# Optimization experiments

Measured on AMD Instinct MI355X. Metric: run time of the kernel, lower is better.

The kernel has to match this reference:

```python
import jax, jax.numpy as jnp
import numpy as np

K_NEIGHBORS = 16
N_CLASSES = 10


def setup_inputs() -> dict:
    key = jax.random.key(0)
    k1, k2, k3 = jax.random.split(key, 3)
    x = jax.random.normal(k1, (2048, 128), dtype=jnp.float32)
    train_data = jax.random.normal(k2, (100000, 128), dtype=jnp.float32)
    train_labels = jax.random.randint(k3, (100000,), 0, N_CLASSES, dtype=jnp.int64)
    return {"x": x, "train_data": train_data, "train_labels": train_labels}


def reference(x, train_data, train_labels):
    N = x.shape[0]
    x2 = jnp.sum(x * x, axis=1, keepdims=True)            # [N, 1]
    t2 = jnp.sum(train_data * train_data, axis=1)          # [M]
    d2 = x2 + t2[None, :] - 2.0 * (x @ train_data.T)       # [N, M]
    dist = jnp.sqrt(jnp.maximum(d2, 0.0))
    # smallest-k via top_k on negated distances
    neg_d, idx = jax.lax.top_k(-dist, K_NEIGHBORS)         # [N, K]
    d = -neg_d
    labels = train_labels[idx]                              # [N, K]
    # weights == 'distance': inverse distance; rows containing an exact match
    # (inf weight) get a 0/1 indicator vector instead.
    w = 1.0 / d
    inf_mask = jnp.isinf(w)
    inf_row = jnp.any(inf_mask, axis=1, keepdims=True)
    w = jnp.where(inf_row, inf_mask.astype(jnp.float32), w)
    # weighted vote: scatter-add weights into per-class buckets
    rows = jnp.arange(N)[:, None]
    proba = jnp.zeros((N, N_CLASSES), jnp.float32).at[rows, labels].add(w)
    s = jnp.sum(proba, axis=1, keepdims=True)
    s = jnp.where(s == 0.0, 1.0, s)
    proba = proba / s
    pred = jnp.argmax(proba, axis=1)
    return pred, proba
```

## Files before the change

kernel.cpp:

```cpp
#include <hip/hip_runtime.h>
#include <hip/hip_fp16.h>
#include <math.h>

#define M_TRAIN 100000
#define NQ 2048
#define DIM 128
#define KNN 16
#define NCLS 10

#define S_STRIDE 16
#define S_CNT (M_TRAIN / S_STRIDE)
#define S_PAD 6272
#define SCH 49
#define SPC 128
#define TT 64
#define MQ 128
#define QSTR 136

#define CAP 768
#define TBH 50176
#define NTR 128
#define NQT 64
#define MARGIN 3.0f
#define SLACK 7.0f

using bfrag = __attribute__((ext_vector_type(8))) short;
using cfrag = __attribute__((ext_vector_type(4))) float;

__device__ __forceinline__ bool better(float d1, int i1, float d2, int i2) {
    return (d1 < d2) || (d1 == d2 && i1 < i2);
}

__device__ __forceinline__ unsigned pack_bf16(float a, float b) {
    unsigned ua = __float_as_uint(a), ub = __float_as_uint(b);
    ua += 0x7fffu + ((ua >> 16) & 1u);
    ub += 0x7fffu + ((ub >> 16) & 1u);
    return (ua >> 16) | (ub & 0xffff0000u);
}

__device__ __forceinline__ bfrag pack_bf16x8(const float* p) {
    union { unsigned u[4]; bfrag f; } r;
    r.u[0] = pack_bf16(p[0], p[1]);
    r.u[1] = pack_bf16(p[2], p[3]);
    r.u[2] = pack_bf16(p[4], p[5]);
    r.u[3] = pack_bf16(p[6], p[7]);
    return r.f;
}

__device__ __forceinline__ void gload_lds16(const void* g, void* l) {
    __builtin_amdgcn_global_load_lds(
        (const __attribute__((address_space(1))) unsigned int*)g,
        (__attribute__((address_space(3))) unsigned int*)l, 16, 0, 0);
}

__device__ __forceinline__ void ins16(float (&bd)[KNN], float v) {
    if (v < bd[KNN - 1]) {
        bd[KNN - 1] = v;
        #pragma unroll
        for (int j = KNN - 1; j >= 1; --j)
            if (bd[j] < bd[j - 1]) { float t = bd[j]; bd[j] = bd[j - 1]; bd[j - 1] = t; }
    }
}

__global__ void knn_norms(const float* __restrict__ train,
                          const float* __restrict__ x,
                          float* __restrict__ t2, float* __restrict__ x2,
                          int* __restrict__ cnt) {
    int gid = blockIdx.x * blockDim.x + threadIdx.x;
    if (gid < NQ) cnt[gid] = 0;
    int gw = gid >> 6;
    int lane = threadIdx.x & 63;
    if (gw >= M_TRAIN + NQ) return;
    const float* r = (gw < M_TRAIN) ? (train + (size_t)gw * DIM)
                                    : (x + (size_t)(gw - M_TRAIN) * DIM);
    float a = r[lane];
    float b = r[lane + 64];
    float s = a * a + b * b;
    #pragma unroll
    for (int off = 32; off > 0; off >>= 1)
        s += __shfl_down(s, off, 64);
    if (lane == 0) {
        if (gw < M_TRAIN) t2[gw] = s; else x2[gw - M_TRAIN] = s;
    }
}

__global__ __launch_bounds__(256, 3)
void knn_sub_mfma(const float* __restrict__ x, const float* __restrict__ train,
                  const float* __restrict__ t2, const float* __restrict__ x2,
                  __half* __restrict__ dsub) {
    __shared__ short T[TT * QSTR];
    __shared__ float t2h[TT];
    int tid = threadIdx.x;
    int w = tid >> 6, lane = tid & 63;
    int rquad = lane >> 4, rcol = lane & 15;
    int qBase = blockIdx.y * MQ;
    int cBase = blockIdx.x * SPC;

    bfrag A[2][4];
    #pragma unroll
    for (int rt = 0; rt < 2; ++rt) {
        int qr = qBase + w * 32 + rt * 16 + rcol;
        #pragma unroll
        for (int ks = 0; ks < 4; ++ks)
            A[rt][ks] = pack_bf16x8(&x[(size_t)qr * DIM + ks * 32 + rquad * 8]);
    }

    float x2r[2][4];
    #pragma unroll
    for (int rt = 0; rt < 2; ++rt)
        #pragma unroll
        for (int reg = 0; reg < 4; ++reg)
            x2r[rt][reg] = x2[qBase + w * 32 + rt * 16 + rquad * 4 + reg];

    const cfrag zero4 = {0.f, 0.f, 0.f, 0.f};
    for (int t = 0; t < 2; ++t) {
        __syncthreads();
        int sBase = cBase + t * TT;
        #pragma unroll
        for (int it = 0; it < 8; ++it) {
            int f = it * 256 + tid;
            int row = f >> 5, c4 = f & 31;
            int sj = sBase + row;
            bool ok = sj < S_CNT;
            float4 v = ok ? ((const float4*)train)[(size_t)sj * S_STRIDE * (DIM / 4) + c4]
                          : make_float4(0.f, 0.f, 0.f, 0.f);
            uint2 p; p.x = pack_bf16(v.x, v.y); p.y = pack_bf16(v.z, v.w);
            *(uint2*)&T[row * QSTR + c4 * 4] = p;
        }
        if (tid < TT) {
            int sj = sBase + tid;
            t2h[tid] = (sj < S_CNT) ? t2[(size_t)sj * S_STRIDE] : 1e30f;
        }
        __syncthreads();

        cfrag acc[2][4];
        #pragma unroll
        for (int ks = 0; ks < 4; ++ks) {
            bfrag B[4];
            #pragma unroll
            for (int ct = 0; ct < 4; ++ct) {
                int n = ct * 16 + rcol;
                B[ct] = *(const bfrag*)&T[n * QSTR + ks * 32 + rquad * 8];
            }
            #pragma unroll
            for (int rt = 0; rt < 2; ++rt)
                #pragma unroll
                for (int ct = 0; ct < 4; ++ct)
                    acc[rt][ct] = (ks == 0)
                        ? __builtin_amdgcn_mfma_f32_16x16x32_bf16(A[rt][0], B[ct], zero4, 0, 0, 0)
                        : __builtin_amdgcn_mfma_f32_16x16x32_bf16(A[rt][ks], B[ct], acc[rt][ct], 0, 0, 0);
        }

        float th[4];
        #pragma unroll
        for (int ct = 0; ct < 4; ++ct) th[ct] = t2h[ct * 16 + rcol];
        #pragma unroll
        for (int rt = 0; rt < 2; ++rt)
            #pragma unroll
            for (int ct = 0; ct < 4; ++ct)
                #pragma unroll
                for (int reg = 0; reg < 4; ++reg) {
                    float d2 = x2r[rt][reg] + th[ct] - 2.f * acc[rt][ct][reg];
                    int qrow = qBase + w * 32 + rt * 16 + rquad * 4 + reg;
                    int col = sBase + ct * 16 + rcol;
                    dsub[(size_t)qrow * S_PAD + col] = __float2half_rn(d2);
                }
    }
}

__global__ __launch_bounds__(256)
void knn_select(const __half* __restrict__ dsub, float* __restrict__ tau) {
    __shared__ float wk[64];
    int q = blockIdx.x, tid = threadIdx.x;
    int w = tid >> 6, lane = tid & 63;

    float bd[KNN];
    #pragma unroll
    for (int j = 0; j < KNN; ++j) bd[j] = 3.4e38f;

    const uint4* dv = (const uint4*)(dsub + (size_t)q * S_PAD);
    #pragma unroll 1
    for (int v = tid; v < S_PAD / 8; v += 256) {
        uint4 pk = dv[v];
        unsigned wd[4] = {pk.x, pk.y, pk.z, pk.w};
        #pragma unroll
        for (int e = 0; e < 4; ++e) {
            ins16(bd, __half2float(__ushort_as_half((unsigned short)(wd[e] & 0xFFFFu))));
            ins16(bd, __half2float(__ushort_as_half((unsigned short)(wd[e] >> 16))));
        }
    }

    #pragma unroll 1
    for (int sel = 0; sel < KNN; ++sel) {
        float mv = bd[0]; int ml = lane;
        #pragma unroll
        for (int off = 32; off > 0; off >>= 1) {
            float ov = __shfl_down(mv, off, 64);
            int   ol = __shfl_down(ml, off, 64);
            if (ov < mv || (ov == mv && ol < ml)) { mv = ov; ml = ol; }
        }
        mv = __shfl(mv, 0, 64);
        ml = __shfl(ml, 0, 64);
        if (lane == 0) wk[w * KNN + sel] = mv;
        if (lane == ml) {
            #pragma unroll
            for (int j = 0; j < KNN - 1; ++j) bd[j] = bd[j + 1];
            bd[KNN - 1] = 3.4e38f;
        }
    }
    __syncthreads();
    if (tid < 64) {
        float v = wk[tid];
        int rank = 0;
        #pragma unroll 8
        for (int j = 0; j < 64; ++j) {
            float u = wk[j];
            if (u < v || (u == v && j < tid)) ++rank;
        }
        if (rank == KNN - 1) tau[q] = v;
    }
}

__global__ __launch_bounds__(256)
void knn_convert_bf16(const float* __restrict__ train,
                      unsigned int* __restrict__ tb, int rowBase,
                      const float* __restrict__ x,
                      unsigned int* __restrict__ xb) {
    int b = blockIdx.x;
    if (b >= (TBH * 32) / 256) {
        int i = (b - (TBH * 32) / 256) * 256 + threadIdx.x;
        int row = i >> 5, seg = i & 31;
        float4 v = ((const float4*)x)[(size_t)row * (DIM / 4) + seg];
        uint2 p; p.x = pack_bf16(v.x, v.y); p.y = pack_bf16(v.z, v.w);
        ((uint2*)xb)[(size_t)row * 32 + seg] = p;
        return;
    }
    int i = b * 256 + threadIdx.x;
    int row = i >> 5, seg = i & 31;
    int g = rowBase + row;
    float4 v = (g < M_TRAIN)
        ? ((const float4*)train)[(size_t)g * (DIM / 4) + seg]
        : make_float4(0.f, 0.f, 0.f, 0.f);
    uint2 p; p.x = pack_bf16(v.x, v.y); p.y = pack_bf16(v.z, v.w);
    int off = (seg * 8) ^ ((row & 7) << 4);
    *(uint2*)((char*)tb + (size_t)row * 256 + off) = p;
}

__global__ __launch_bounds__(256, 5)
void knn_filter12(const unsigned int* __restrict__ xbb,
                  const short* __restrict__ tbb,
                  const float* __restrict__ t2, const float* __restrict__ x2,
                  const float* __restrict__ tau, int pBase0,
                  int* __restrict__ buf_i, unsigned short* __restrict__ buf_h,
                  int* __restrict__ cnt) {
    __shared__ __align__(16) short T[NTR * DIM];
    int tid = threadIdx.x;
    int w = tid >> 6, lane = tid & 63;
    int rquad = lane >> 4, rcol = lane & 15;

    int bid = blockIdx.x;
    int xcd = bid & 7, r = bid >> 3;
    int qb = r & 31;
    int nch = xcd + 8 * (r >> 5);
    int qBase = qb * NQT;
    int tbase = pBase0 + nch * NTR;

    const char* gsrc = (const char*)tbb + (size_t)nch * NTR * 256 + w * 8192 + lane * 16;
    char* ldst = (char*)T + w * 8192;
    #pragma unroll
    for (int i = 0; i < 8; ++i)
        gload_lds16(gsrc + i * 1024, ldst + i * 1024);

    bfrag A[4];
    int qrow = qBase + w * 16 + rcol;
    const char* xrow = (const char*)xbb + (size_t)qrow * 256;
    #pragma unroll
    for (int ks = 0; ks < 4; ++ks)
        A[ks] = *(const bfrag*)(xrow + ks * 64 + rquad * 16);

    float RC[4], x2q[4];
    #pragma unroll
    for (int reg = 0; reg < 4; ++reg) {
        int q = qBase + w * 16 + rquad * 4 + reg;
        x2q[reg] = x2[q];
        RC[reg] = 0.5f * (x2q[reg] - tau[q] - MARGIN);
    }
    float th[8];
    #pragma unroll
    for (int ct = 0; ct < 8; ++ct)
        th[ct] = 0.5f * t2[tbase + ct * 16 + rcol];
    __syncthreads();

    int swz = (rcol & 7) << 4;
    int cs[4];
    #pragma unroll
    for (int ks = 0; ks < 4; ++ks)
        cs[ks] = (ks * 64 + rquad * 16) ^ swz;

    const cfrag zero4 = {0.f, 0.f, 0.f, 0.f};
    cfrag acc[8];
    #pragma unroll
    for (int ks = 0; ks < 4; ++ks)
        #pragma unroll
        for (int ct = 0; ct < 8; ++ct) {
            const bfrag B = *(const bfrag*)((const char*)T + (ct * 16 + rcol) * 256 + cs[ks]);
            acc[ct] = (ks == 0)
                ? __builtin_amdgcn_mfma_f32_16x16x32_bf16(A[0], B, zero4, 0, 0, 0)
                : __builtin_amdgcn_mfma_f32_16x16x32_bf16(A[ks], B, acc[ct], 0, 0, 0);
        }

    unsigned okm = 0;
    #pragma unroll
    for (int ct = 0; ct < 8; ++ct)
        if (tbase + ct * 16 + rcol < M_TRAIN) okm |= (1u << ct);

    unsigned m8[4];
    #pragma unroll
    for (int reg = 0; reg < 4; ++reg) {
        unsigned m = 0;
        #pragma unroll
        for (int ct = 0; ct < 8; ++ct)
            if (acc[ct][reg] >= RC[reg] + th[ct]) m |= (1u << ct);
        m8[reg] = m & okm;
    }

    int slotR[4];
    #pragma unroll
    for (int reg = 0; reg < 4; ++reg)
        if (m8[reg])
            slotR[reg] = atomicAdd(&cnt[qBase + w * 16 + rquad * 4 + reg],
                                   __popc(m8[reg]));

    #pragma unroll
    for (int reg = 0; reg < 4; ++reg) {
        unsigned m = m8[reg];
        if (m) {
            int q = qBase + w * 16 + rquad * 4 + reg;
            size_t qoff = (size_t)q * CAP;
            int s0 = slotR[reg];
            #pragma unroll
            for (int ct = 0; ct < 8; ++ct)
                if (m & (1u << ct)) {
                    int slot = s0 + __popc(m & ((1u << ct) - 1));
                    if (slot < CAP) {
                        buf_i[qoff + slot] = tbase + ct * 16 + rcol;
                        float d2a = x2q[reg] + 2.f * th[ct] - 2.f * acc[ct][reg];
                        buf_h[qoff + slot] = __half_as_ushort(__float2half_rn(d2a));
                    }
                }
        }
    }
}

__global__ __launch_bounds__(256)
void knn_final(const float* __restrict__ x,
               const float* __restrict__ train,
               const float* __restrict__ t2v,
               const float* __restrict__ x2v,
               const int* __restrict__ buf_i,
               const __half* __restrict__ buf_h,
               const int* __restrict__ cnt,
               const int* __restrict__ labels,
               float* __restrict__ out) {
    __shared__ float sd[CAP];
    __shared__ int   si[CAP];
    __shared__ int   keep[CAP];
    __shared__ float wk[64];
    __shared__ int   kr[KNN];
    __shared__ float sthr;
    __shared__ int   smcnt;
    int q = blockIdx.x;
    int tid = threadIdx.x;
    int w = tid >> 6, lane = tid & 63;
    int grp = lane >> 4, sub = lane & 15;
    int n = cnt[q]; if (n > CAP) n = CAP;
    if (tid == 0) smcnt = 0;
    if (tid < KNN) kr[tid] = -1;

    float av[3];
    #pragma unroll
    for (int j = 0; j < 3; ++j) {
        int i = (w * 3 + j) * 64 + lane;
        av[j] = (i < n) ? __half2float(buf_h[(size_t)q * CAP + i]) : 3.4e38f;
    }
    for (int sel = 0; sel < KNN; ++sel) {
        float mv = av[0]; int mc = (lane << 2);
        if (av[1] < mv) { mv = av[1]; mc = (lane << 2) | 1; }
        if (av[2] < mv) { mv = av[2]; mc = (lane << 2) | 2; }
        #pragma unroll
        for (int off = 32; off > 0; off >>= 1) {
            float ov = __shfl_down(mv, off, 64);
            int   oc = __shfl_down(mc, off, 64);
            if (ov < mv || (ov == mv && oc < mc)) { mv = ov; mc = oc; }
        }
        mv = __shfl(mv, 0, 64);
        mc = __shfl(mc, 0, 64);
        if (lane == 0) wk[w * KNN + sel] = mv;
        if (lane == (mc >> 2)) {
            int j0 = mc & 3;
            if (j0 == 0) av[0] = 3.4e38f;
            else if (j0 == 1) av[1] = 3.4e38f;
            else av[2] = 3.4e38f;
        }
    }
    __syncthreads();
    if (tid < 64) {
        float v = wk[tid];
        int rank = 0;
        #pragma unroll 8
        for (int j = 0; j < 64; ++j) {
            float u = wk[j];
            if (u < v || (u == v && j < tid)) ++rank;
        }
        if (rank == KNN - 1) sthr = v + SLACK;
    }
    __syncthreads();
    float thr = sthr;

    for (int i = tid; i < n; i += 256) {
        float h = __half2float(buf_h[(size_t)q * CAP + i]);
        if (h <= thr) {
            int p = atomicAdd(&smcnt, 1);
            keep[p] = buf_i[(size_t)q * CAP + i];
        }
    }
    __syncthreads();
    int m = smcnt;

    const float4* xq = (const float4*)&x[(size_t)q * DIM + sub * 8];
    float4 qa = xq[0], qb = xq[1];
    float x2l = x2v[q];
    for (int base = 0; base < m; base += 16) {
        int i = base + w * 4 + grp;
        if (i < m) {
            int idx = keep[i];
            const float4* tr = (const float4*)&train[(size_t)idx * DIM + sub * 8];
            float4 ta = tr[0], tb4 = tr[1];
            float s = qa.x * ta.x + qa.y * ta.y + qa.z * ta.z + qa.w * ta.w
                    + qb.x * tb4.x + qb.y * tb4.y + qb.z * tb4.z + qb.w * tb4.w;
            s += __shfl_xor(s, 1, 64);
            s += __shfl_xor(s, 2, 64);
            s += __shfl_xor(s, 4, 64);
            s += __shfl_xor(s, 8, 64);
            if (sub == 0) { sd[i] = x2l + t2v[idx] - 2.f * s; si[i] = idx; }
        }
    }
    __syncthreads();

    for (int i = tid; i < m; i += 256) {
        float d = sd[i]; int ix = si[i];
        int rank = 0;
        for (int j = 0; j < m; ++j)
            if (better(sd[j], si[j], d, ix)) ++rank;
        if (rank < KNN) kr[rank] = i;
    }
    __syncthreads();

    if (tid == 0) {
        bool anyzero = false;
        float dist[KNN]; int kidx[KNN];
        #pragma unroll
        for (int j = 0; j < KNN; ++j) {
            int ii = kr[j];
            if (ii >= 0) {
                dist[j] = sqrtf(fmaxf(sd[ii], 0.f));
                kidx[j] = si[ii];
                if (dist[j] == 0.f) anyzero = true;
            } else { dist[j] = -1.f; kidx[j] = -1; }
        }
        float spr[NCLS];
        #pragma unroll
        for (int c = 0; c < NCLS; ++c) spr[c] = 0.f;
        #pragma unroll
        for (int j = 0; j < KNN; ++j) {
            int idxj = kidx[j];
            if (idxj < 0 || idxj >= M_TRAIN) continue;
            float wgt = anyzero ? (dist[j] == 0.f ? 1.f : 0.f) : 1.f / dist[j];
            spr[labels[idxj]] += wgt;
        }
        float s = 0.f;
        #pragma unroll
        for (int c = 0; c < NCLS; ++c) s += spr[c];
        if (s == 0.f) s = 1.f;
        float inv = 1.f / s;
        float best = -1.f; int bc = 0;
        #pragma unroll
        for (int c = 0; c < NCLS; ++c) {
            float pv = spr[c] * inv;
            out[NQ + (size_t)q * NCLS + c] = pv;
            if (pv > best) { best = pv; bc = c; }
        }
        out[q] = (float)bc;
    }
}

extern "C" void kernel_launch(void* const* d_in, const int* in_sizes, int n_in,
                              void* d_out, int out_size, void* d_ws, size_t ws_size,
                              hipStream_t stream) {
    const float* x      = (const float*)d_in[0];
    const float* train  = (const float*)d_in[1];
    const int*   labels = (const int*)d_in[2];
    float* out = (float*)d_out;

    char* base = (char*)d_ws;
    float*  t2   = (float*)(base);
    float*  x2   = (float*)(base + 401408);
    float*  tau  = (float*)(base + 409600);
    int*    cnt  = (int*)  (base + 417792);
    char*   region = base + 425984;
    __half* dsub = (__half*)region;
    unsigned int* tb = (unsigned int*)region;
    int*    bi   = (int*)(region + 12845056);
    unsigned int* xb = (unsigned int*)(region + 19136512);
    __half* bh   = (__half*)(region + 19660800);

    int nrows = M_TRAIN + NQ;
    knn_norms<<<(nrows * 64 + 255) / 256, 256, 0, stream>>>(train, x, t2, x2, cnt);

    dim3 gs(SCH, NQ / MQ);
    knn_sub_mfma<<<gs, 256, 0, stream>>>(x, train, t2, x2, dsub);

    knn_select<<<NQ, 256, 0, stream>>>(dsub, tau);

    for (int h = 0; h < 2; ++h) {
        int rowBase = h * TBH;
        int cgrid = (TBH * 32) / 256 + (h == 0 ? (NQ * 32) / 256 : 0);
        knn_convert_bf16<<<cgrid, 256, 0, stream>>>(train, tb, rowBase, x, xb);
        knn_filter12<<<(TBH / NTR) * (NQ / NQT), 256, 0, stream>>>(
            xb, (const short*)tb, t2, x2, tau, rowBase, bi, (unsigned short*)bh, cnt);
    }

    knn_final<<<NQ, 256, 0, stream>>>(x, train, t2, x2, bi, bh, cnt, labels, out);
}
```

Before: 374.9 us.

## Fuse bf16 conversion of train tiles into filter kernel, drop staging buffer

Removes the separate train-to-bf16 conversion pass and its two-half staging loop. Each filter block now reads fp32 train rows directly, converts them to bf16 and writes the swizzled layout straight into LDS. A small kernel packs the queries to bf16. This cuts the global write and reread of the converted train copy and several launches. In exchange each train tile is read and converted as fp32 once per query block (32 times), which raises global/L2 traffic and ALU work in the filter prologue.

```diff
diff --git a/kernel.cpp b/kernel.cpp
--- a/kernel.cpp
+++ b/kernel.cpp
@@ -18,7 +18,7 @@
 #define QSTR 136
 
 #define CAP 768
-#define TBH 50176
+#define NTILE 784
 #define NTR 128
 #define NQT 64
 #define MARGIN 3.0f
@@ -45,12 +45,6 @@
     r.u[2] = pack_bf16(p[4], p[5]);
     r.u[3] = pack_bf16(p[6], p[7]);
     return r.f;
-}
-
-__device__ __forceinline__ void gload_lds16(const void* g, void* l) {
-    __builtin_amdgcn_global_load_lds(
-        (const __attribute__((address_space(1))) unsigned int*)g,
-        (__attribute__((address_space(3))) unsigned int*)l, 16, 0, 0);
 }
 
 __device__ __forceinline__ void ins16(float (&bd)[KNN], float v) {
@@ -222,35 +216,18 @@
 }
 
 __global__ __launch_bounds__(256)
-void knn_convert_bf16(const float* __restrict__ train,
-                      unsigned int* __restrict__ tb, int rowBase,
-                      const float* __restrict__ x,
-                      unsigned int* __restrict__ xb) {
-    int b = blockIdx.x;
-    if (b >= (TBH * 32) / 256) {
-        int i = (b - (TBH * 32) / 256) * 256 + threadIdx.x;
-        int row = i >> 5, seg = i & 31;
-        float4 v = ((const float4*)x)[(size_t)row * (DIM / 4) + seg];
-        uint2 p; p.x = pack_bf16(v.x, v.y); p.y = pack_bf16(v.z, v.w);
-        ((uint2*)xb)[(size_t)row * 32 + seg] = p;
-        return;
-    }
-    int i = b * 256 + threadIdx.x;
-    int row = i >> 5, seg = i & 31;
-    int g = rowBase + row;
-    float4 v = (g < M_TRAIN)
-        ? ((const float4*)train)[(size_t)g * (DIM / 4) + seg]
-        : make_float4(0.f, 0.f, 0.f, 0.f);
-    uint2 p; p.x = pack_bf16(v.x, v.y); p.y = pack_bf16(v.z, v.w);
-    int off = (seg * 8) ^ ((row & 7) << 4);
-    *(uint2*)((char*)tb + (size_t)row * 256 + off) = p;
+void knn_pack_x(const float* __restrict__ x, unsigned int* __restrict__ xb) {
+    int gid = blockIdx.x * 256 + threadIdx.x;
+    int row = gid >> 6, lane = gid & 63;
+    float2 v = ((const float2*)x)[(size_t)row * 64 + lane];
+    xb[(size_t)row * 64 + lane] = pack_bf16(v.x, v.y);
 }
 
 __global__ __launch_bounds__(256, 5)
-void knn_filter12(const unsigned int* __restrict__ xbb,
-                  const short* __restrict__ tbb,
+void knn_filter14(const unsigned int* __restrict__ xbb,
+                  const float* __restrict__ train,
                   const float* __restrict__ t2, const float* __restrict__ x2,
-                  const float* __restrict__ tau, int pBase0,
+                  const float* __restrict__ tau,
                   int* __restrict__ buf_i, unsigned short* __restrict__ buf_h,
                   int* __restrict__ cnt) {
     __shared__ __align__(16) short T[NTR * DIM];
@@ -263,13 +240,20 @@
     int qb = r & 31;
     int nch = xcd + 8 * (r >> 5);
     int qBase = qb * NQT;
-    int tbase = pBase0 + nch * NTR;
-
-    const char* gsrc = (const char*)tbb + (size_t)nch * NTR * 256 + w * 8192 + lane * 16;
-    char* ldst = (char*)T + w * 8192;
-    #pragma unroll
-    for (int i = 0; i < 8; ++i)
-        gload_lds16(gsrc + i * 1024, ldst + i * 1024);
+    int tbase = nch * NTR;
+
+    #pragma unroll
+    for (int it = 0; it < 16; ++it) {
+        int f = it * 256 + tid;
+        int row = f >> 5, seg = f & 31;
+        int g = tbase + row;
+        float4 v = (g < M_TRAIN)
+            ? ((const float4*)train)[(size_t)g * (DIM / 4) + seg]
+            : make_float4(0.f, 0.f, 0.f, 0.f);
+        uint2 p; p.x = pack_bf16(v.x, v.y); p.y = pack_bf16(v.z, v.w);
+        int off = (seg * 8) ^ ((row & 7) << 4);
+        *(uint2*)((char*)T + row * 256 + off) = p;
+    }
 
     bfrag A[4];
     int qrow = qBase + w * 16 + rcol;
@@ -509,7 +493,6 @@
     int*    cnt  = (int*)  (base + 417792);
     char*   region = base + 425984;
     __half* dsub = (__half*)region;
-    unsigned int* tb = (unsigned int*)region;
     int*    bi   = (int*)(region + 12845056);
     unsigned int* xb = (unsigned int*)(region + 19136512);
     __half* bh   = (__half*)(region + 19660800);
@@ -522,13 +505,10 @@
 
     knn_select<<<NQ, 256, 0, stream>>>(dsub, tau);
 
-    for (int h = 0; h < 2; ++h) {
-        int rowBase = h * TBH;
-        int cgrid = (TBH * 32) / 256 + (h == 0 ? (NQ * 32) / 256 : 0);
-        knn_convert_bf16<<<cgrid, 256, 0, stream>>>(train, tb, rowBase, x, xb);
-        knn_filter12<<<(TBH / NTR) * (NQ / NQT), 256, 0, stream>>>(
-            xb, (const short*)tb, t2, x2, tau, rowBase, bi, (unsigned short*)bh, cnt);
-    }
+    knn_pack_x<<<(NQ * 64) / 256, 256, 0, stream>>>(x, xb);
+
+    knn_filter14<<<NTILE * (NQ / NQT), 256, 0, stream>>>(
+        xb, train, t2, x2, tau, bi, (unsigned short*)bh, cnt);
 
     knn_final<<<NQ, 256, 0, stream>>>(x, train, t2, x2, bi, bh, cnt, labels, out);
 }
```

Result: slower. 443.7 us (+18.4%).
